# Kernel tuning notes

Hardware: AMD Instinct MI355X
Metric: run time of the kernel (lower is better)

Reference implementation:

```python
import jax, jax.numpy as jnp
import numpy as np
from jax import lax

TAGSET = 48
START_TAG = 46
STOP_TAG = 47
B, T = 128, 256

def setup_inputs() -> dict:
    key = jax.random.key(0)
    k1, k2, k3 = jax.random.split(key, 3)
    features = jax.random.normal(k1, (B, T, TAGSET, TAGSET), dtype=jnp.float32)
    targets = jax.random.randint(k2, (B, T), 0, TAGSET * TAGSET, dtype=jnp.int64)
    # lengths in [1, T], sorted descending as pack_padded_sequence expects
    lengths = jnp.sort(jax.random.randint(k3, (B,), 1, T + 1, dtype=jnp.int64))[::-1]
    return {"features": features, "targets": targets, "lengths": lengths}

def reference(features, targets, lengths):
    b, t, k, _ = features.shape
    # gold score: gather flattened (from_tag*K + to_tag) scores, sum over valid timesteps
    gathered = jnp.take_along_axis(
        features.reshape(b, t, k * k), targets[..., None], axis=2
    ).squeeze(-1)  # (B, T)
    valid = jnp.arange(t)[None, :] < lengths[:, None]  # (B, T) bool
    gold_score = jnp.sum(jnp.where(valid, gathered, 0.0))

    # forward algorithm: t=0 initializes from START_TAG row (all lengths >= 1)
    init = features[:, 0, START_TAG, :]  # (B, K)

    def step(scores_upto_t, inputs):
        feats_t, mask_t = inputs  # (B, K, K), (B,)
        upd = jax.nn.logsumexp(feats_t + scores_upto_t[:, :, None], axis=1)  # lse over from-tag
        new = jnp.where(mask_t[:, None], upd, scores_upto_t)  # freeze finished sequences
        return new, None

    feats_rest = jnp.swapaxes(features[:, 1:], 0, 1)  # (T-1, B, K, K)
    mask_rest = jnp.swapaxes(valid[:, 1:], 0, 1)      # (T-1, B)
    final, _ = lax.scan(step, init, (feats_rest, mask_rest))
    all_paths_scores = final[:, STOP_TAG].sum()
    return all_paths_scores - gold_score
```

## Files before the change

### kernel.cpp

```cpp
#include <hip/hip_runtime.h>


#define NB 128
#define NT 256
#define NK 48
#define NKK (NK * NK)
#define TAG_START 46
#define TAG_STOP 47
#define PFD 4

#define STEP_BARRIER() asm volatile("s_waitcnt lgkmcnt(0)\n\ts_barrier" ::: "memory")

__device__ __forceinline__ float dpp_xor1(float x) {
    return __int_as_float(__builtin_amdgcn_update_dpp(
        0, __float_as_int(x), 0xB1, 0xF, 0xF, true));
}
__device__ __forceinline__ float dpp_xor2(float x) {
    return __int_as_float(__builtin_amdgcn_update_dpp(
        0, __float_as_int(x), 0x4E, 0xF, 0xF, true));
}

#define LD12(v, p, ST) \
  v##0 = (p)[0*(ST)];  v##1 = (p)[1*(ST)];  v##2  = (p)[2*(ST)];  v##3  = (p)[3*(ST)]; \
  v##4 = (p)[4*(ST)];  v##5 = (p)[5*(ST)];  v##6  = (p)[6*(ST)];  v##7  = (p)[7*(ST)]; \
  v##8 = (p)[8*(ST)];  v##9 = (p)[9*(ST)];  v##10 = (p)[10*(ST)]; v##11 = (p)[11*(ST)];

#define STEPB(v, ST) { \
  const float* sc_ = &sv[(u + 1) & 1][rb]; \
  float4 s0 = *(const float4*)(sc_);     \
  float4 s1 = *(const float4*)(sc_ + 4); \
  float4 s2 = *(const float4*)(sc_ + 8); \
  if (((u - 1) & 3) == 0) { \
    float mm = fmaxf(fmaxf(fmaxf(s0.x,s0.y),fmaxf(s0.z,s0.w)), \
                     fmaxf(fmaxf(s1.x,s1.y),fmaxf(s1.z,s1.w))); \
    mm = fmaxf(mm, fmaxf(fmaxf(s2.x,s2.y),fmaxf(s2.z,s2.w))); \
    mm = fmaxf(mm, dpp_xor1(mm)); \
    mm = fmaxf(mm, dpp_xor2(mm)); \
    c += mm; \
    s0.x-=mm; s0.y-=mm; s0.z-=mm; s0.w-=mm; \
    s1.x-=mm; s1.y-=mm; s1.z-=mm; s1.w-=mm; \
    s2.x-=mm; s2.y-=mm; s2.z-=mm; s2.w-=mm; \
  } \
  float acc = (((__expf(v##0 + s0.x) + __expf(v##1 + s0.y)) + \
                (__expf(v##2 + s0.z) + __expf(v##3 + s0.w))) + \
               ((__expf(v##4 + s1.x) + __expf(v##5 + s1.y)) + \
                (__expf(v##6 + s1.z) + __expf(v##7 + s1.w)))) + \
              ((__expf(v##8 + s2.x) + __expf(v##9 + s2.y)) + \
               (__expf(v##10 + s2.z) + __expf(v##11 + s2.w))); \
  acc += dpp_xor1(acc); \
  acc += dpp_xor2(acc); \
  if (store) sv[u & 1][oo] = __logf(acc); \
  { int up_ = u + PFD; if (up_ > nsteps) up_ = nsteps; \
    const float* p_ = basep + (long)up_ * dstep; LD12(v, p_, ST) } \
  STEP_BARRIER(); \
}

#define CHAIN(ST) { \
  float a0,a1,a2,a3,a4,a5,a6,a7,a8,a9,a10,a11; \
  float b0,b1,b2,b3,b4,b5,b6,b7,b8,b9,b10,b11; \
  float c0,c1,c2,c3,c4,c5,c6,c7,c8,c9,c10,c11; \
  float d0,d1,d2,d3,d4,d5,d6,d7,d8,d9,d10,d11; \
  { const float* p_ = basep + dstep; LD12(a, p_, ST) } \
  { int up_ = (2 > nsteps) ? nsteps : 2; \
    const float* p_ = basep + (long)up_ * dstep; LD12(b, p_, ST) } \
  { int up_ = (3 > nsteps) ? nsteps : 3; \
    const float* p_ = basep + (long)up_ * dstep; LD12(c, p_, ST) } \
  { int up_ = (4 > nsteps) ? nsteps : 4; \
    const float* p_ = basep + (long)up_ * dstep; LD12(d, p_, ST) } \
  __syncthreads(); \
  int u = 1; \
  for (;;) { \
    STEPB(a, ST) \
    if (++u > nsteps) break; \
    STEPB(b, ST) \
    if (++u > nsteps) break; \
    STEPB(c, ST) \
    if (++u > nsteps) break; \
    STEPB(d, ST) \
    if (++u > nsteps) break; \
  } \
}

__global__ __launch_bounds__(256, 1)
void viterbi_chain_kernel(const float* __restrict__ feats,
                          const int* __restrict__ targets,
                          const int* __restrict__ lengths,
                          float* __restrict__ out,
                          float* __restrict__ ws)
{
    const int bu  = blockIdx.x;
    const int b   = bu >> 1;
    const int dir = bu & 1;
    const int tid = threadIdx.x;
    const int len = lengths[b], last = len - 1, m = last >> 1;
    const float* __restrict__ fb = feats + (size_t)b * (NT * NKK);

    __shared__ float sv[2][NK];
    __shared__ float gred[4];

    {
        int tg  = dir ? (m + 1 + tid) : tid;
        int tmx = dir ? last : m;
        float g = 0.f;
        if (tg <= tmx) g = fb[(size_t)tg * NKK + targets[b * NT + tg]];
        #pragma unroll
        for (int o = 32; o; o >>= 1) g += __shfl_down(g, o, 64);
        if ((tid & 63) == 0) gred[tid >> 6] = g;
    }

    if (tid < NK) {
        float iv;
        if (dir) iv = (last == 0) ? ((tid == TAG_STOP) ? 0.f : -1e30f)
                                  : fb[(size_t)last * NKK + tid * NK + TAG_STOP];
        else     iv = fb[TAG_START * NK + tid];
        sv[0][tid] = iv;
    }

    const int lane = tid & 63, w = tid >> 6, qq = lane & 3, rb = qq * 12;
    const int oo   = w * 12 + (lane >> 2);
    const int ooc  = (oo < NK) ? oo : (NK - 1);
    const bool store = ((lane >> 2) < 12) && (qq == 0);

    int nsteps = dir ? (last - 1 - m) : m;
    if (nsteps < 0) nsteps = 0;

    float c = 0.f;
    if (nsteps > 0) {
        if (dir) {
            const float* basep = fb + (size_t)last * NKK + (size_t)ooc * NK + rb;
            const long dstep = -(long)NKK;
            CHAIN(1)
        } else {
            const float* basep = fb + (size_t)rb * NK + ooc;
            const long dstep = (long)NKK;
            CHAIN(NK)
        }
    } else {
        __syncthreads();
    }

    if (tid < NK) ws[(size_t)bu * 64 + tid] = sv[nsteps & 1][tid];
    if (tid == 0) {
        ws[(size_t)bu * 64 + 48] = c;
        atomicAdd(out, -(gred[0] + gred[1] + gred[2] + gred[3]));
    }
}

__global__ __launch_bounds__(64, 1)
void viterbi_combine_kernel(const float* __restrict__ ws,
                            float* __restrict__ out)
{
    const int b = blockIdx.x, lane = threadIdx.x;
    const float* f = ws + (size_t)(2 * b) * 64;
    const float* g = ws + (size_t)(2 * b + 1) * 64;
    float v = -3.0e38f;
    if (lane < NK) v = f[lane] + g[lane];
    float mm = v;
    #pragma unroll
    for (int o = 32; o; o >>= 1) mm = fmaxf(mm, __shfl_xor(mm, o, 64));
    float e = (lane < NK) ? __expf(v - mm) : 0.f;
    #pragma unroll
    for (int o = 32; o; o >>= 1) e += __shfl_xor(e, o, 64);
    if (lane == 0) atomicAdd(out, __logf(e) + mm + f[NK] + g[NK]);
}

extern "C" void kernel_launch(void* const* d_in, const int* in_sizes, int n_in,
                              void* d_out, int out_size, void* d_ws, size_t ws_size,
                              hipStream_t stream) {
    const float* feats   = (const float*)d_in[0];
    const int*   targets = (const int*)d_in[1];
    const int*   lengths = (const int*)d_in[2];
    float*       out     = (float*)d_out;
    float*       ws      = (float*)d_ws;

    hipMemsetAsync(out, 0, sizeof(float), stream);
    viterbi_chain_kernel<<<dim3(2 * NB), dim3(NT), 0, stream>>>(feats, targets, lengths, out, ws);
    viterbi_combine_kernel<<<dim3(NB), dim3(64), 0, stream>>>(ws, out);
}
```

Baseline: 416.9 us.

## Run each chain half in a single wavefront using readlane broadcast instead of LDS barriers

Each block now has one 64-lane wavefront in place of four. Each lane owns one output tag and loops over all 48 source tags, with the running score vector broadcast through readlane instead of shared memory. This removes the per-step LDS store, barrier and DPP cross-lane reductions. It also moves to base-2 exp/log with a per-step readfirstlane renormalisation, and prefetches three steps ahead with 48-register buffers. The cost is 4x more exp work per lane, much higher register pressure, and less memory-level parallelism per block.

```diff
diff --git a/kernel.cpp b/kernel.cpp
--- a/kernel.cpp
+++ b/kernel.cpp
@@ -7,142 +7,131 @@
 #define NKK (NK * NK)
 #define TAG_START 46
 #define TAG_STOP 47
-#define PFD 4
+#define K_LOG2E 1.4426950408889634f
+#define K_LN2   0.6931471805599453f
 
-#define STEP_BARRIER() asm volatile("s_waitcnt lgkmcnt(0)\n\ts_barrier" ::: "memory")
+#define DECL48(v) \
+  float v##0,v##1,v##2,v##3,v##4,v##5,v##6,v##7,v##8,v##9,v##10,v##11, \
+        v##12,v##13,v##14,v##15,v##16,v##17,v##18,v##19,v##20,v##21,v##22,v##23, \
+        v##24,v##25,v##26,v##27,v##28,v##29,v##30,v##31,v##32,v##33,v##34,v##35, \
+        v##36,v##37,v##38,v##39,v##40,v##41,v##42,v##43,v##44,v##45,v##46,v##47;
 
-__device__ __forceinline__ float dpp_xor1(float x) {
-    return __int_as_float(__builtin_amdgcn_update_dpp(
-        0, __float_as_int(x), 0xB1, 0xF, 0xF, true));
-}
-__device__ __forceinline__ float dpp_xor2(float x) {
-    return __int_as_float(__builtin_amdgcn_update_dpp(
-        0, __float_as_int(x), 0x4E, 0xF, 0xF, true));
+#define LD48C(v, p) \
+  v##0 =(p)[0*NK];  v##1 =(p)[1*NK];  v##2 =(p)[2*NK];  v##3 =(p)[3*NK]; \
+  v##4 =(p)[4*NK];  v##5 =(p)[5*NK];  v##6 =(p)[6*NK];  v##7 =(p)[7*NK]; \
+  v##8 =(p)[8*NK];  v##9 =(p)[9*NK];  v##10=(p)[10*NK]; v##11=(p)[11*NK]; \
+  v##12=(p)[12*NK]; v##13=(p)[13*NK]; v##14=(p)[14*NK]; v##15=(p)[15*NK]; \
+  v##16=(p)[16*NK]; v##17=(p)[17*NK]; v##18=(p)[18*NK]; v##19=(p)[19*NK]; \
+  v##20=(p)[20*NK]; v##21=(p)[21*NK]; v##22=(p)[22*NK]; v##23=(p)[23*NK]; \
+  v##24=(p)[24*NK]; v##25=(p)[25*NK]; v##26=(p)[26*NK]; v##27=(p)[27*NK]; \
+  v##28=(p)[28*NK]; v##29=(p)[29*NK]; v##30=(p)[30*NK]; v##31=(p)[31*NK]; \
+  v##32=(p)[32*NK]; v##33=(p)[33*NK]; v##34=(p)[34*NK]; v##35=(p)[35*NK]; \
+  v##36=(p)[36*NK]; v##37=(p)[37*NK]; v##38=(p)[38*NK]; v##39=(p)[39*NK]; \
+  v##40=(p)[40*NK]; v##41=(p)[41*NK]; v##42=(p)[42*NK]; v##43=(p)[43*NK]; \
+  v##44=(p)[44*NK]; v##45=(p)[45*NK]; v##46=(p)[46*NK]; v##47=(p)[47*NK];
+
+#define LD48R(v, p) { \
+  const float4* q_ = (const float4*)(p); \
+  float4 r0_=q_[0], r1_=q_[1], r2_ =q_[2],  r3_ =q_[3]; \
+  float4 r4_=q_[4], r5_=q_[5], r6_ =q_[6],  r7_ =q_[7]; \
+  float4 r8_=q_[8], r9_=q_[9], r10_=q_[10], r11_=q_[11]; \
+  v##0 =r0_.x;  v##1 =r0_.y;  v##2 =r0_.z;  v##3 =r0_.w; \
+  v##4 =r1_.x;  v##5 =r1_.y;  v##6 =r1_.z;  v##7 =r1_.w; \
+  v##8 =r2_.x;  v##9 =r2_.y;  v##10=r2_.z;  v##11=r2_.w; \
+  v##12=r3_.x;  v##13=r3_.y;  v##14=r3_.z;  v##15=r3_.w; \
+  v##16=r4_.x;  v##17=r4_.y;  v##18=r4_.z;  v##19=r4_.w; \
+  v##20=r5_.x;  v##21=r5_.y;  v##22=r5_.z;  v##23=r5_.w; \
+  v##24=r6_.x;  v##25=r6_.y;  v##26=r6_.z;  v##27=r6_.w; \
+  v##28=r7_.x;  v##29=r7_.y;  v##30=r7_.z;  v##31=r7_.w; \
+  v##32=r8_.x;  v##33=r8_.y;  v##34=r8_.z;  v##35=r8_.w; \
+  v##36=r9_.x;  v##37=r9_.y;  v##38=r9_.z;  v##39=r9_.w; \
+  v##40=r10_.x; v##41=r10_.y; v##42=r10_.z; v##43=r10_.w; \
+  v##44=r11_.x; v##45=r11_.y; v##46=r11_.z; v##47=r11_.w; }
+
+#define RL(i) __int_as_float(__builtin_amdgcn_readlane(__float_as_int(s2), (i)))
+#define TT(v,i) exp2f(__builtin_fmaf(v##i, K_LOG2E, RL(i)))
+
+#define SUMTREE48(v) \
+ ((((((TT(v,0)+TT(v,1))+(TT(v,2)+TT(v,3)))+((TT(v,4)+TT(v,5))+(TT(v,6)+TT(v,7)))) + \
+    (((TT(v,8)+TT(v,9))+(TT(v,10)+TT(v,11)))+((TT(v,12)+TT(v,13))+(TT(v,14)+TT(v,15))))) + \
+   ((((TT(v,16)+TT(v,17))+(TT(v,18)+TT(v,19)))+((TT(v,20)+TT(v,21))+(TT(v,22)+TT(v,23)))) + \
+    (((TT(v,24)+TT(v,25))+(TT(v,26)+TT(v,27)))+((TT(v,28)+TT(v,29))+(TT(v,30)+TT(v,31)))))) + \
+  ((((TT(v,32)+TT(v,33))+(TT(v,34)+TT(v,35)))+((TT(v,36)+TT(v,37))+(TT(v,38)+TT(v,39)))) + \
+   (((TT(v,40)+TT(v,41))+(TT(v,42)+TT(v,43)))+((TT(v,44)+TT(v,45))+(TT(v,46)+TT(v,47))))))
+
+#define STEP48(v, LDM) { \
+  float acc_ = SUMTREE48(v); \
+  { int up_ = u + 3; if (up_ > nsteps) up_ = nsteps; \
+    const float* p_ = basep + (long)up_ * dstep; LDM(v, p_) } \
+  float l2_ = __log2f(acc_); \
+  float d2_ = __int_as_float(__builtin_amdgcn_readfirstlane(__float_as_int(l2_))); \
+  s2 = l2_ - d2_; \
+  c  = __builtin_fmaf(d2_, K_LN2, c); \
 }
 
-#define LD12(v, p, ST) \
-  v##0 = (p)[0*(ST)];  v##1 = (p)[1*(ST)];  v##2  = (p)[2*(ST)];  v##3  = (p)[3*(ST)]; \
-  v##4 = (p)[4*(ST)];  v##5 = (p)[5*(ST)];  v##6  = (p)[6*(ST)];  v##7  = (p)[7*(ST)]; \
-  v##8 = (p)[8*(ST)];  v##9 = (p)[9*(ST)];  v##10 = (p)[10*(ST)]; v##11 = (p)[11*(ST)];
-
-#define STEPB(v, ST) { \
-  const float* sc_ = &sv[(u + 1) & 1][rb]; \
-  float4 s0 = *(const float4*)(sc_);     \
-  float4 s1 = *(const float4*)(sc_ + 4); \
-  float4 s2 = *(const float4*)(sc_ + 8); \
-  if (((u - 1) & 3) == 0) { \
-    float mm = fmaxf(fmaxf(fmaxf(s0.x,s0.y),fmaxf(s0.z,s0.w)), \
-                     fmaxf(fmaxf(s1.x,s1.y),fmaxf(s1.z,s1.w))); \
-    mm = fmaxf(mm, fmaxf(fmaxf(s2.x,s2.y),fmaxf(s2.z,s2.w))); \
-    mm = fmaxf(mm, dpp_xor1(mm)); \
-    mm = fmaxf(mm, dpp_xor2(mm)); \
-    c += mm; \
-    s0.x-=mm; s0.y-=mm; s0.z-=mm; s0.w-=mm; \
-    s1.x-=mm; s1.y-=mm; s1.z-=mm; s1.w-=mm; \
-    s2.x-=mm; s2.y-=mm; s2.z-=mm; s2.w-=mm; \
-  } \
-  float acc = (((__expf(v##0 + s0.x) + __expf(v##1 + s0.y)) + \
-                (__expf(v##2 + s0.z) + __expf(v##3 + s0.w))) + \
-               ((__expf(v##4 + s1.x) + __expf(v##5 + s1.y)) + \
-                (__expf(v##6 + s1.z) + __expf(v##7 + s1.w)))) + \
-              ((__expf(v##8 + s2.x) + __expf(v##9 + s2.y)) + \
-               (__expf(v##10 + s2.z) + __expf(v##11 + s2.w))); \
-  acc += dpp_xor1(acc); \
-  acc += dpp_xor2(acc); \
-  if (store) sv[u & 1][oo] = __logf(acc); \
-  { int up_ = u + PFD; if (up_ > nsteps) up_ = nsteps; \
-    const float* p_ = basep + (long)up_ * dstep; LD12(v, p_, ST) } \
-  STEP_BARRIER(); \
-}
-
-#define CHAIN(ST) { \
-  float a0,a1,a2,a3,a4,a5,a6,a7,a8,a9,a10,a11; \
-  float b0,b1,b2,b3,b4,b5,b6,b7,b8,b9,b10,b11; \
-  float c0,c1,c2,c3,c4,c5,c6,c7,c8,c9,c10,c11; \
-  float d0,d1,d2,d3,d4,d5,d6,d7,d8,d9,d10,d11; \
-  { const float* p_ = basep + dstep; LD12(a, p_, ST) } \
+#define CHAIN48(LDM) { \
+  DECL48(A) DECL48(B) DECL48(C) \
+  { const float* p_ = basep + dstep; LDM(A, p_) } \
   { int up_ = (2 > nsteps) ? nsteps : 2; \
-    const float* p_ = basep + (long)up_ * dstep; LD12(b, p_, ST) } \
+    const float* p_ = basep + (long)up_ * dstep; LDM(B, p_) } \
   { int up_ = (3 > nsteps) ? nsteps : 3; \
-    const float* p_ = basep + (long)up_ * dstep; LD12(c, p_, ST) } \
-  { int up_ = (4 > nsteps) ? nsteps : 4; \
-    const float* p_ = basep + (long)up_ * dstep; LD12(d, p_, ST) } \
-  __syncthreads(); \
+    const float* p_ = basep + (long)up_ * dstep; LDM(C, p_) } \
   int u = 1; \
   for (;;) { \
-    STEPB(a, ST) \
-    if (++u > nsteps) break; \
-    STEPB(b, ST) \
-    if (++u > nsteps) break; \
-    STEPB(c, ST) \
-    if (++u > nsteps) break; \
-    STEPB(d, ST) \
-    if (++u > nsteps) break; \
+    STEP48(A, LDM) if (++u > nsteps) break; \
+    STEP48(B, LDM) if (++u > nsteps) break; \
+    STEP48(C, LDM) if (++u > nsteps) break; \
   } \
 }
 
-__global__ __launch_bounds__(256, 1)
+__global__ __launch_bounds__(64, 1)
 void viterbi_chain_kernel(const float* __restrict__ feats,
                           const int* __restrict__ targets,
                           const int* __restrict__ lengths,
                           float* __restrict__ out,
                           float* __restrict__ ws)
 {
-    const int bu  = blockIdx.x;
-    const int b   = bu >> 1;
-    const int dir = bu & 1;
-    const int tid = threadIdx.x;
+    const int bu   = blockIdx.x;
+    const int b    = bu >> 1;
+    const int dir  = bu & 1;
+    const int lane = threadIdx.x;
     const int len = lengths[b], last = len - 1, m = last >> 1;
     const float* __restrict__ fb = feats + (size_t)b * (NT * NKK);
 
-    __shared__ float sv[2][NK];
-    __shared__ float gred[4];
-
+    float gold = 0.f;
     {
-        int tg  = dir ? (m + 1 + tid) : tid;
+        int t   = dir ? (m + 1 + lane) : lane;
         int tmx = dir ? last : m;
-        float g = 0.f;
-        if (tg <= tmx) g = fb[(size_t)tg * NKK + targets[b * NT + tg]];
+        while (t <= tmx) { gold += fb[(size_t)t * NKK + targets[b * NT + t]]; t += 64; }
         #pragma unroll
-        for (int o = 32; o; o >>= 1) g += __shfl_down(g, o, 64);
-        if ((tid & 63) == 0) gred[tid >> 6] = g;
+        for (int o = 32; o; o >>= 1) gold += __shfl_down(gold, o, 64);
     }
 
-    if (tid < NK) {
-        float iv;
-        if (dir) iv = (last == 0) ? ((tid == TAG_STOP) ? 0.f : -1e30f)
-                                  : fb[(size_t)last * NKK + tid * NK + TAG_STOP];
-        else     iv = fb[TAG_START * NK + tid];
-        sv[0][tid] = iv;
-    }
-
-    const int lane = tid & 63, w = tid >> 6, qq = lane & 3, rb = qq * 12;
-    const int oo   = w * 12 + (lane >> 2);
-    const int ooc  = (oo < NK) ? oo : (NK - 1);
-    const bool store = ((lane >> 2) < 12) && (qq == 0);
-
+    const int ooc = (lane < NK) ? lane : (NK - 1);
     int nsteps = dir ? (last - 1 - m) : m;
     if (nsteps < 0) nsteps = 0;
 
-    float c = 0.f;
+    float s2, c = 0.f;
+    if (dir) s2 = (last == 0) ? ((ooc == TAG_STOP) ? 0.f : -1e30f)
+                              : fb[(size_t)last * NKK + (size_t)ooc * NK + TAG_STOP] * K_LOG2E;
+    else     s2 = fb[TAG_START * NK + ooc] * K_LOG2E;
+
     if (nsteps > 0) {
         if (dir) {
-            const float* basep = fb + (size_t)last * NKK + (size_t)ooc * NK + rb;
+            const float* basep = fb + (size_t)last * NKK + (size_t)ooc * NK;
             const long dstep = -(long)NKK;
-            CHAIN(1)
+            CHAIN48(LD48R)
         } else {
-            const float* basep = fb + (size_t)rb * NK + ooc;
+            const float* basep = fb + ooc;
             const long dstep = (long)NKK;
-            CHAIN(NK)
+            CHAIN48(LD48C)
         }
-    } else {
-        __syncthreads();
     }
 
-    if (tid < NK) ws[(size_t)bu * 64 + tid] = sv[nsteps & 1][tid];
-    if (tid == 0) {
+    if (lane < NK) ws[(size_t)bu * 64 + lane] = s2 * K_LN2;
+    if (lane == 0) {
         ws[(size_t)bu * 64 + 48] = c;
-        atomicAdd(out, -(gred[0] + gred[1] + gred[2] + gred[3]));
+        atomicAdd(out, -gold);
     }
 }
 
@@ -174,6 +163,6 @@
     float*       ws      = (float*)d_ws;
 
     hipMemsetAsync(out, 0, sizeof(float), stream);
-    viterbi_chain_kernel<<<dim3(2 * NB), dim3(NT), 0, stream>>>(feats, targets, lengths, out, ws);
+    viterbi_chain_kernel<<<dim3(2 * NB), dim3(64), 0, stream>>>(feats, targets, lengths, out, ws);
     viterbi_combine_kernel<<<dim3(NB), dim3(64), 0, stream>>>(ws, out);
 }
```

Measured after the change: 506.9 us. +21.6%, slower.
